# Optimization experiments

Measured on AMD Instinct MI355X. Metric: run time of the kernel, lower is better.

Reference implementation:

```python
import jax, jax.numpy as jnp
import numpy as np

DIM = 1024
TOPK = 64
PAIRS = DIM // 2  # phase_pairs default
PHASE_MIX = 0.5
GATE_THRESHOLD = 0.0
EPS = 1e-12  # F.normalize default eps


def _l2norm(v):
    # matches F.normalize(v, dim=-1): v / max(||v||, eps)
    n = jnp.linalg.norm(v, axis=-1, keepdims=True)
    return v / jnp.maximum(n, EPS)


def setup_inputs() -> dict:
    key = jax.random.key(0)
    ks = jax.random.split(key, 6)
    s = 0.02  # small init scale for weights
    return {
        "x": jax.random.normal(ks[0], (4, 4096, DIM), dtype=jnp.float32),
        "gate_W": jax.random.normal(ks[1], (DIM, DIM), dtype=jnp.float32) * s,
        "gate_b": jnp.zeros((DIM,), dtype=jnp.float32),
        "mag_W": jax.random.normal(ks[2], (DIM, DIM), dtype=jnp.float32) * s,
        "mag_b": jnp.zeros((DIM,), dtype=jnp.float32),
        "Wq": jax.random.normal(ks[3], (DIM, DIM), dtype=jnp.float32) * s,
        "Wk": jax.random.normal(ks[4], (DIM, DIM), dtype=jnp.float32) * s,
        "phase_W": jax.random.normal(ks[5], (2 * PAIRS, DIM), dtype=jnp.float32) * s,
    }


def reference(x, gate_W, gate_b, mag_W, mag_b, Wq, Wk, phase_W):
    B, S, D = x.shape
    # gated SAE-style projection (gated=True, diag=False)
    gate_pre = x @ gate_W.T + gate_b          # [B,S,D]
    mag_pre = x @ mag_W.T + mag_b             # [B,S,D]
    # hard gate with straight-through estimator
    gate_soft = jax.nn.sigmoid(gate_pre)
    gate_hard = (gate_pre > GATE_THRESHOLD).astype(x.dtype)
    gate = gate_hard + gate_soft - jax.lax.stop_gradient(gate_soft)
    mag = jax.nn.relu(mag_pre)
    # top-k scatter mask along feature dim
    idx = jax.lax.top_k(gate_pre, TOPK)[1]    # [B,S,K]
    rows = jnp.arange(B * S)[:, None]
    mask = (jnp.zeros((B * S, D), dtype=bool)
            .at[rows, idx.reshape(B * S, TOPK)].set(True)
            .reshape(B, S, D))
    gate = jnp.where(mask, gate, jnp.zeros_like(gate))
    mag = jnp.where(mask, mag, jnp.zeros_like(mag))
    xg = gate * mag
    # twist projections, L2-normalized
    q = _l2norm(xg @ Wq.T)
    k = _l2norm(xg @ Wk.T)
    # symplectic momentum map over consecutive steps
    momentum_map = q[:, 1:] * k[:, :-1] - q[:, :-1] * k[:, 1:]  # [B,S-1,D]
    twist_mag = jnp.linalg.norm(momentum_map, axis=-1, keepdims=True)
    complexity = jnp.pad(jnp.tanh(twist_mag), ((0, 0), (1, 0), (0, 0)))  # [B,S,1]
    # phase branch (phase_mix > 0)
    phase = (xg @ phase_W.T).reshape(B, S, PAIRS, 2)
    phase = _l2norm(phase)
    pp, pc = phase[:, :-1], phase[:, 1:]
    cross = pp[..., 0] * pc[..., 1] - pp[..., 1] * pc[..., 0]   # [B,S-1,P]
    dot = jnp.clip(jnp.sum(pp * pc, axis=-1), -1.0, 1.0)
    phase_delta = jnp.abs(jnp.arctan2(cross, dot)) / jnp.pi
    phase_score = jnp.pad(jnp.mean(phase_delta, axis=-1, keepdims=True),
                          ((0, 0), (1, 0), (0, 0)))             # [B,S,1]
    return (1.0 - PHASE_MIX) * complexity + PHASE_MIX * phase_score
```

## Files before the change

kernel.cpp:

```cpp
#include <hip/hip_runtime.h>
#include <math.h>

#define DIM 1024
#define ROWS 16384
#define SEQ 4096
#define MARGIN 0.012f
#define MAXC 24

typedef __bf16 v8bf __attribute__((ext_vector_type(8)));
typedef float v4f __attribute__((ext_vector_type(4)));
typedef int v8i __attribute__((ext_vector_type(8)));

__device__ __forceinline__ unsigned short f2bf(float f){
  unsigned u = __float_as_uint(f);
  u = u + 0x7FFFu + ((u >> 16) & 1u);
  return (unsigned short)(u >> 16);
}
__device__ __forceinline__ float bf2f(unsigned short h){
  return __uint_as_float(((unsigned)h) << 16);
}
__device__ __forceinline__ unsigned short relu_bf(unsigned short h){
  return (h & 0x8000u) ? (unsigned short)0 : h;
}
__device__ __forceinline__ unsigned f2fp8(float f){
  float a = fabsf(f);
  unsigned sign = (__float_as_uint(f) >> 24) & 0x80u;
  if (a >= 448.f) return sign | 0x7Eu;
  if (a < 0.015625f){
    int k = (int)rintf(a * 512.f);
    if (k >= 8) return sign | 0x08u;
    return sign | (unsigned)k;
  }
  unsigned u = __float_as_uint(a);
  u += 0x7FFFFu + ((u >> 20) & 1u);
  int e = (int)((u >> 23) & 0xFFu) - 127;
  unsigned m = (u >> 20) & 7u;
  if (e > 8) return sign | 0x7Eu;
  return sign | ((unsigned)(e + 7) << 3) | m;
}
__device__ __forceinline__ void lds_fence(){
  __asm__ volatile("s_waitcnt lgkmcnt(0)" ::: "memory");
}

__global__ __launch_bounds__(256) void cvt_all(
    const float* __restrict__ x,
    const float* __restrict__ w0, const float* __restrict__ w1,
    const float* __restrict__ w2, const float* __restrict__ w3,
    const float* __restrict__ w4,
    unsigned short* __restrict__ xbf, unsigned short* __restrict__ wbf,
    unsigned char* __restrict__ wf8){
  const int y = blockIdx.y;
  int i = (blockIdx.x * 256 + threadIdx.x) * 4;
  if (y < 16){
    const float* s = x + ((size_t)y << 20);
    float4 f = *(const float4*)(s + i);
    ushort4 o; o.x = f2bf(f.x); o.y = f2bf(f.y); o.z = f2bf(f.z); o.w = f2bf(f.w);
    *(ushort4*)(xbf + ((size_t)y << 20) + i) = o;
  } else if (y < 18){
    const float* s = (y == 16) ? w0 : w1;
    float4 f = *(const float4*)(s + i);
    ushort4 o; o.x = f2bf(f.x); o.y = f2bf(f.y); o.z = f2bf(f.z); o.w = f2bf(f.w);
    *(ushort4*)(wbf + ((size_t)(y - 16) << 20) + i) = o;
  } else {
    const float* s = (y == 18) ? w2 : ((y == 19) ? w3 : w4);
    float4 f = *(const float4*)(s + i);
    unsigned u = f2fp8(f.x * 32.f) | (f2fp8(f.y * 32.f) << 8) |
                 (f2fp8(f.z * 32.f) << 16) | (f2fp8(f.w * 32.f) << 24);
    *(unsigned*)(wf8 + ((size_t)(y - 18) << 20) + i) = u;
  }
}

#define GBAR() asm volatile("s_barrier" ::: "memory")
#define GLGKM0() { asm volatile("s_waitcnt lgkmcnt(0)" ::: "memory"); __builtin_amdgcn_sched_barrier(0); }
#define GVM4() asm volatile("s_waitcnt vmcnt(4)" ::: "memory")

__global__ __launch_bounds__(512, 2) void gemm_bt(
    const unsigned short* __restrict__ A, const unsigned short* __restrict__ B,
    const float* __restrict__ bias0, const float* __restrict__ bias1,
    unsigned short* __restrict__ C0, unsigned short* __restrict__ C1)
{
  extern __shared__ unsigned char lds[];
  const int t = threadIdx.x;
  const int lane = t & 63, wave = t >> 6;
  const int wr = wave >> 2, wc = wave & 3;
  const int bid = blockIdx.x;
  const int swz = (bid & 7) * 64 + (bid >> 3);
  const int m0 = (swz & 63) * 256;
  const int n0 = (swz >> 6) * 256;

  int offv[4];
#pragma unroll
  for (int h = 0; h < 2; h++)
#pragma unroll
    for (int i = 0; i < 2; i++){
      int o = h * 16384 + i * 8192 + t * 16;
      int u = o ^ (((o >> 9) & 1) << 5);
      int r = ((u >> 11) << 4) | ((u >> 6) & 15);
      int c = (((u >> 10) & 1) << 5) | ((u & 63) >> 1);
      offv[h * 2 + i] = r * 1024 + c;
    }
  const int off00 = offv[0], off01 = offv[1], off10 = offv[2], off11 = offv[3];
  const unsigned short* Ab = A + ((size_t)m0 << 10);
  const unsigned short* Bb = B + ((size_t)n0 << 10);

  const int laneterm = (lane & 15) * 64 + (((lane >> 4) * 16) ^ (((lane >> 3) & 1) * 32));
  const int aBase = wr * 16384 + laneterm;
  const int bBase = 32768 + wc * 8192 + laneterm;

#define GLD1(srcp, dsto) __builtin_amdgcn_global_load_lds( \
    (const __attribute__((address_space(1))) void*)(srcp), \
    (__attribute__((address_space(3))) void*)(lds + (dsto)), 16, 0, 0)

  auto stageA = [&](int h, int kt, int pp){
    const int o0 = h ? off10 : off00, o1 = h ? off11 : off01;
    GLD1(Ab + o0 + kt * 64, pp * 65536 + h * 16384 + t * 16);
    GLD1(Ab + o1 + kt * 64, pp * 65536 + h * 16384 + 8192 + t * 16);
  };
  auto stageB = [&](int h, int kt, int pp){
    const int o0 = h ? off10 : off00, o1 = h ? off11 : off01;
    GLD1(Bb + o0 + kt * 64, pp * 65536 + 32768 + h * 16384 + t * 16);
    GLD1(Bb + o1 + kt * 64, pp * 65536 + 32768 + h * 16384 + 8192 + t * 16);
  };

  v4f acc[8][4];
#pragma unroll
  for (int i = 0; i < 8; i++)
#pragma unroll
    for (int j = 0; j < 4; j++) acc[i][j] = v4f{0.f, 0.f, 0.f, 0.f};

  stageB(0, 0, 0); stageB(1, 0, 0);
  stageA(0, 0, 0); stageA(1, 0, 0);
  stageB(0, 1, 1); stageB(1, 1, 1);
  GVM4();
  GBAR();

  int p = 0;
  for (int X = 0; X < 16; X++, p ^= 1){
    const int pb = p * 65536;
    const int ktA = (X + 1 < 16) ? X + 1 : 15;
    const int ktB = (X + 2 < 16) ? X + 2 : X;
    v8bf a0[8], a1[8], b0[4], b1[4];

#pragma unroll
    for (int mi = 0; mi < 8; mi++) a0[mi] = *(const v8bf*)(lds + pb + aBase + mi * 2048);
#pragma unroll
    for (int ni = 0; ni < 4; ni++) b0[ni] = *(const v8bf*)(lds + pb + bBase + ni * 2048);
    stageA(0, ktA, p ^ 1);
    GBAR();
    __builtin_amdgcn_s_setprio(1);
#pragma unroll
    for (int mi = 0; mi < 4; mi++)
#pragma unroll
      for (int ni = 0; ni < 4; ni++)
        acc[mi][ni] = __builtin_amdgcn_mfma_f32_16x16x32_bf16(a0[mi], b0[ni], acc[mi][ni], 0, 0, 0);
    __builtin_amdgcn_s_setprio(0);
    GBAR();

#pragma unroll
    for (int mi = 0; mi < 4; mi++) a1[mi] = *(const v8bf*)(lds + pb + aBase + 1024 + mi * 2048);
#pragma unroll
    for (int ni = 0; ni < 4; ni++) b1[ni] = *(const v8bf*)(lds + pb + bBase + 1024 + ni * 2048);
    stageA(1, ktA, p ^ 1);
    GBAR();
    __builtin_amdgcn_s_setprio(1);
#pragma unroll
    for (int mi = 0; mi < 4; mi++)
#pragma unroll
      for (int ni = 0; ni < 4; ni++)
        acc[4 + mi][ni] = __builtin_amdgcn_mfma_f32_16x16x32_bf16(a0[4 + mi], b0[ni], acc[4 + mi][ni], 0, 0, 0);
    __builtin_amdgcn_s_setprio(0);
    GLGKM0();
    GBAR();

#pragma unroll
    for (int mi = 4; mi < 8; mi++) a1[mi] = *(const v8bf*)(lds + pb + aBase + 1024 + mi * 2048);
    stageB(0, ktB, p);
    GBAR();
    __builtin_amdgcn_s_setprio(1);
#pragma unroll
    for (int mi = 0; mi < 4; mi++)
#pragma unroll
      for (int ni = 0; ni < 4; ni++)
        acc[mi][ni] = __builtin_amdgcn_mfma_f32_16x16x32_bf16(a1[mi], b1[ni], acc[mi][ni], 0, 0, 0);
    __builtin_amdgcn_s_setprio(0);
    GBAR();

    stageB(1, ktB, p);
    GBAR();
    __builtin_amdgcn_s_setprio(1);
#pragma unroll
    for (int mi = 0; mi < 4; mi++)
#pragma unroll
      for (int ni = 0; ni < 4; ni++)
        acc[4 + mi][ni] = __builtin_amdgcn_mfma_f32_16x16x32_bf16(a1[4 + mi], b1[ni], acc[4 + mi][ni], 0, 0, 0);
    __builtin_amdgcn_s_setprio(0);
    GVM4();
    GBAR();
  }

  asm volatile("s_waitcnt vmcnt(0)" ::: "memory");
  __syncthreads();

  const int os = n0 >> 10;
  unsigned short* Cp = (os == 0) ? C0 : C1;
  const float* bp = (os == 0) ? bias0 : bias1;
  const int colbase = n0 & (DIM - 1);
  unsigned short* lt = (unsigned short*)lds;
  const int ar = lane & 15, aq = lane >> 4;
  const int lrw = wr * 16 + aq * 4;
  const int lrow = t >> 4;
  const int cseg = (t & 15) * 16;
  const size_t grb = (size_t)(m0 + (lrow >> 4) * 128 + (lrow & 15)) * DIM + colbase + cseg;
  float bv[4];
#pragma unroll
  for (int ni = 0; ni < 4; ni++) bv[ni] = bp[colbase + wc * 64 + ni * 16 + ar];
#pragma unroll
  for (int mi = 0; mi < 8; mi++){
#pragma unroll
    for (int ni = 0; ni < 4; ni++){
      const int colc = wc * 64 + ni * 16 + ar;
#pragma unroll
      for (int rr = 0; rr < 4; rr++)
        lt[(lrw + rr) * 264 + colc] = f2bf(acc[mi][ni][rr] + bv[ni]);
    }
    __syncthreads();
    uint4 v0 = *(const uint4*)&lt[lrow * 264 + cseg];
    uint4 v1 = *(const uint4*)&lt[lrow * 264 + cseg + 8];
    *(uint4*)(Cp + grb + (size_t)mi * 16 * DIM) = v0;
    *(uint4*)(Cp + grb + (size_t)mi * 16 * DIM + 8) = v1;
    __syncthreads();
  }
  asm volatile("s_waitcnt vmcnt(0)" ::: "memory");
}

__global__ __launch_bounds__(256, 3) void gemm8(
    const unsigned char* __restrict__ A, const unsigned char* __restrict__ B,
    unsigned short* __restrict__ C0, unsigned short* __restrict__ C1,
    unsigned short* __restrict__ C2)
{
  __shared__ unsigned char lA[128 * 128];
  __shared__ unsigned char lB[128 * 128];
  const int t = threadIdx.x;
  const int lane = t & 63, wave = t >> 6;
  const int bid0 = blockIdx.y * gridDim.x + blockIdx.x;
  const int swz = (bid0 & 7) * 384 + (bid0 >> 3);
  const int m0 = (swz & 127) * 128;
  const int n0 = (swz >> 7) * 128;
  const int wm = (wave >> 1) * 64, wn = (wave & 1) * 64;
  const int ar = lane & 15, aq = lane >> 4;

  v4f acc[4][4];
#pragma unroll
  for (int i = 0; i < 4; i++)
#pragma unroll
    for (int j = 0; j < 4; j++) acc[i][j] = v4f{0.f, 0.f, 0.f, 0.f};

  for (int k0 = 0; k0 < DIM; k0 += 128){
#pragma unroll
    for (int i = 0; i < 4; i++){
      int c = (wave * 4 + i) * 64 + lane;
      int row = c >> 3, kq = c & 7;
      __builtin_amdgcn_global_load_lds(
        (const __attribute__((address_space(1))) void*)(A + (size_t)(m0 + row) * DIM + k0 + kq * 16),
        (__attribute__((address_space(3))) void*)(&lA[c * 16]), 16, 0, 0);
      __builtin_amdgcn_global_load_lds(
        (const __attribute__((address_space(1))) void*)(B + (size_t)(n0 + row) * DIM + k0 + kq * 16),
        (__attribute__((address_space(3))) void*)(&lB[c * 16]), 16, 0, 0);
    }
    __syncthreads();
    v8i a8[4], b8[4];
#pragma unroll
    for (int i = 0; i < 4; i++){
      a8[i] = *(const v8i*)&lA[(wm + i * 16 + ar) * 128 + aq * 32];
      b8[i] = *(const v8i*)&lB[(wn + i * 16 + ar) * 128 + aq * 32];
    }
#pragma unroll
    for (int mi = 0; mi < 4; mi++)
#pragma unroll
      for (int ni = 0; ni < 4; ni++)
        acc[mi][ni] = __builtin_amdgcn_mfma_scale_f32_16x16x128_f8f6f4(
            a8[mi], b8[ni], acc[mi][ni], 0, 0, 0, 127u, 0, 127u);
    __syncthreads();
  }

  const int os = n0 >> 10;
  unsigned short* Cp = (os == 0) ? C0 : ((os == 1) ? C1 : C2);
  const int colbase = n0 & (DIM - 1);
  unsigned short* lt = (unsigned short*)lA;
  const int lrw = (wave >> 1) * 16 + aq * 4;
  const int colc0 = (wave & 1) * 64;
  const int lrow = t >> 3;
  const int cseg = (t & 7) * 16;
  const size_t grb = (size_t)(m0 + (lrow >> 4) * 64 + (lrow & 15)) * DIM + colbase + cseg;
#pragma unroll
  for (int mi = 0; mi < 4; mi++){
#pragma unroll
    for (int ni = 0; ni < 4; ni++){
      const int colc = colc0 + ni * 16 + ar;
#pragma unroll
      for (int rr = 0; rr < 4; rr++)
        lt[(lrw + rr) * 136 + colc] = f2bf(acc[mi][ni][rr] * 0.03125f);
    }
    __syncthreads();
    uint4 v0 = *(const uint4*)&lt[lrow * 136 + cseg];
    uint4 v1 = *(const uint4*)&lt[lrow * 136 + cseg + 8];
    *(uint4*)(Cp + grb + (size_t)mi * 16 * DIM) = v0;
    *(uint4*)(Cp + grb + (size_t)mi * 16 * DIM + 8) = v1;
    __syncthreads();
  }
}

__global__ __launch_bounds__(256) void select_k(
  const unsigned short* __restrict__ gate_pre, const unsigned short* __restrict__ mag_pre,
  const float* __restrict__ x, const float* __restrict__ gW, const float* __restrict__ gb,
  unsigned char* __restrict__ xg8)
{
  __shared__ int   s_cnt[4];
  __shared__ int   s_idx[4][MAXC];
  __shared__ float s_ex [4][MAXC];
  __shared__ int   s_res[4][MAXC];

  const int t = threadIdx.x;
  const int lane = t & 63, wave = t >> 6;
  const int r = blockIdx.x * 4 + wave;
  const size_t rb = (size_t)r * DIM;

  float vg[16], vx[16];
  unsigned short mg[16];
#pragma unroll
  for (int c = 0; c < 4; c++){
    ushort4 g4 = *(const ushort4*)(gate_pre + rb + c * 256 + lane * 4);
    float4 x4 = *(const float4*)(x          + rb + c * 256 + lane * 4);
    ushort4 m4 = *(const ushort4*)(mag_pre  + rb + c * 256 + lane * 4);
    vg[c*4+0]=bf2f(g4.x); vg[c*4+1]=bf2f(g4.y); vg[c*4+2]=bf2f(g4.z); vg[c*4+3]=bf2f(g4.w);
    vx[c*4+0]=x4.x; vx[c*4+1]=x4.y; vx[c*4+2]=x4.z; vx[c*4+3]=x4.w;
    mg[c*4+0]=m4.x; mg[c*4+1]=m4.y; mg[c*4+2]=m4.z; mg[c*4+3]=m4.w;
  }
  if (lane == 0) s_cnt[wave] = 0;

  float lo = -8.f, hi = 8.f;
#pragma unroll
  for (int it = 0; it < 15; it++){
    float mid = 0.5f * (lo + hi);
    int cn = 0;
#pragma unroll
    for (int e = 0; e < 16; e++) cn += (vg[e] > mid) ? 1 : 0;
#pragma unroll
    for (int m = 32; m; m >>= 1) cn += __shfl_xor(cn, m);
    if (cn >= 64) lo = mid; else hi = mid;
  }
  const float cl = lo - MARGIN, ch = hi + MARGIN;

  int n1 = 0;
#pragma unroll
  for (int e = 0; e < 16; e++) n1 += (vg[e] > ch) ? 1 : 0;
#pragma unroll
  for (int m = 32; m; m >>= 1) n1 += __shfl_xor(n1, m);
  const int s = 64 - n1;

  lds_fence();
#pragma unroll
  for (int e = 0; e < 16; e++){
    float vv = vg[e];
    if (vv >= cl && vv <= ch){
      int p = atomicAdd(&s_cnt[wave], 1);
      if (p < MAXC) s_idx[wave][p] = (e >> 2) * 256 + lane * 4 + (e & 3);
    }
  }
  lds_fence();
  int namb = s_cnt[wave]; if (namb > MAXC) namb = MAXC;

  for (int i = 0; i < namb; i++){
    int d = s_idx[wave][i];
    const float* wr = gW + (size_t)d * DIM;
    float p = 0.f;
#pragma unroll
    for (int c = 0; c < 4; c++){
      float4 w4 = *(const float4*)(wr + c * 256 + lane * 4);
      p = fmaf(vx[c*4+0], w4.x, p); p = fmaf(vx[c*4+1], w4.y, p);
      p = fmaf(vx[c*4+2], w4.z, p); p = fmaf(vx[c*4+3], w4.w, p);
    }
#pragma unroll
    for (int m = 32; m; m >>= 1) p += __shfl_xor(p, m);
    if (lane == 0) s_ex[wave][i] = p + gb[d];
  }
  lds_fence();

  if (lane < namb){
    float e = s_ex[wave][lane]; int d = s_idx[wave][lane];
    int rank = 0;
    for (int j = 0; j < namb; j++){
      float ej = s_ex[wave][j]; int dj = s_idx[wave][j];
      if (ej > e || (ej == e && dj < d)) rank++;
    }
    s_res[wave][lane] = (rank < s && e > 0.f) ? 1 : 0;
  }
  lds_fence();

  float vals[16];
#pragma unroll
  for (int e = 0; e < 16; e++)
    vals[e] = (vg[e] > ch && vg[e] > 0.f) ? bf2f(relu_bf(mg[e])) : 0.f;
  for (int i = 0; i < namb; i++){
    int d = s_idx[wave][i];
    int res = s_res[wave][i];
    if (((d >> 2) & 63) == lane){
      int e = (d >> 8) * 4 + (d & 3);
      vals[e] = res ? bf2f(relu_bf(mg[e])) : 0.f;
    }
  }
#pragma unroll
  for (int c = 0; c < 4; c++){
    unsigned u = f2fp8(vals[c*4+0]) | (f2fp8(vals[c*4+1]) << 8) |
                 (f2fp8(vals[c*4+2]) << 16) | (f2fp8(vals[c*4+3]) << 24);
    *(unsigned*)(xg8 + rb + c * 256 + lane * 4) = u;
  }
}

__global__ __launch_bounds__(256) void epilogue_k(
  const unsigned short* __restrict__ q_pre, const unsigned short* __restrict__ k_pre,
  const unsigned short* __restrict__ p_pre, float* __restrict__ out)
{
  const int r0 = blockIdx.x * 4;
  const int t = threadIdx.x;
  const int lane = t & 63, wave = t >> 6;
  __shared__ float red[16];

  const int rp = (r0 == 0) ? 0 : r0 - 1;
  float vqp[4], vkp[4], vpp[4];
  {
    ushort4 uq = *(const ushort4*)(q_pre + (size_t)rp * DIM + 4*t);
    ushort4 uk = *(const ushort4*)(k_pre + (size_t)rp * DIM + 4*t);
    ushort4 up = *(const ushort4*)(p_pre + (size_t)rp * DIM + 4*t);
    vqp[0]=bf2f(uq.x); vqp[1]=bf2f(uq.y); vqp[2]=bf2f(uq.z); vqp[3]=bf2f(uq.w);
    vkp[0]=bf2f(uk.x); vkp[1]=bf2f(uk.y); vkp[2]=bf2f(uk.z); vkp[3]=bf2f(uk.w);
    vpp[0]=bf2f(up.x); vpp[1]=bf2f(up.y); vpp[2]=bf2f(up.z); vpp[3]=bf2f(up.w);
  }
  float aq = 0.f, ak = 0.f;
#pragma unroll
  for (int j = 0; j < 4; j++){ aq = fmaf(vqp[j], vqp[j], aq); ak = fmaf(vkp[j], vkp[j], ak); }
#pragma unroll
  for (int m = 32; m; m >>= 1){ aq += __shfl_xor(aq, m); ak += __shfl_xor(ak, m); }
  if (lane == 0){ red[wave] = aq; red[4 + wave] = ak; }
  __syncthreads();
  float rqp = 1.f / fmaxf(sqrtf(red[0] + red[1] + red[2] + red[3]), 1e-12f);
  float rkp = 1.f / fmaxf(sqrtf(red[4] + red[5] + red[6] + red[7]), 1e-12f);
  __syncthreads();

  for (int rr = 0; rr < 4; rr++){
    const int r = r0 + rr;
    float vqc[4], vkc[4], vpc[4];
    {
      ushort4 uq = *(const ushort4*)(q_pre + (size_t)r * DIM + 4*t);
      ushort4 uk = *(const ushort4*)(k_pre + (size_t)r * DIM + 4*t);
      ushort4 up = *(const ushort4*)(p_pre + (size_t)r * DIM + 4*t);
      vqc[0]=bf2f(uq.x); vqc[1]=bf2f(uq.y); vqc[2]=bf2f(uq.z); vqc[3]=bf2f(uq.w);
      vkc[0]=bf2f(uk.x); vkc[1]=bf2f(uk.y); vkc[2]=bf2f(uk.z); vkc[3]=bf2f(uk.w);
      vpc[0]=bf2f(up.x); vpc[1]=bf2f(up.y); vpc[2]=bf2f(up.z); vpc[3]=bf2f(up.w);
    }
    const bool seg = (r & (SEQ - 1)) == 0;
    float aqc = 0.f, akc = 0.f;
#pragma unroll
    for (int j = 0; j < 4; j++){ aqc = fmaf(vqc[j], vqc[j], aqc); akc = fmaf(vkc[j], vkc[j], akc); }
    float dsum = 0.f;
    if (!seg){
#pragma unroll
      for (int j = 0; j < 2; j++){
        float ax = vpp[2*j], ay = vpp[2*j+1], bx = vpc[2*j], by = vpc[2*j+1];
        float ia = 1.f / fmaxf(sqrtf(ax * ax + ay * ay), 1e-12f);
        float ib = 1.f / fmaxf(sqrtf(bx * bx + by * by), 1e-12f);
        ax *= ia; ay *= ia; bx *= ib; by *= ib;
        float cross = ax * by - ay * bx;
        float dot = fminf(fmaxf(ax * bx + ay * by, -1.f), 1.f);
        dsum += fabsf(atan2f(cross, dot)) * 0.3183098861837907f;
      }
    }
#pragma unroll
    for (int m = 32; m; m >>= 1){
      aqc += __shfl_xor(aqc, m); akc += __shfl_xor(akc, m); dsum += __shfl_xor(dsum, m);
    }
    if (lane == 0){ red[wave] = aqc; red[4 + wave] = akc; red[8 + wave] = dsum; }
    __syncthreads();
    float rqc = 1.f / fmaxf(sqrtf(red[0] + red[1] + red[2] + red[3]), 1e-12f);
    float rkc = 1.f / fmaxf(sqrtf(red[4] + red[5] + red[6] + red[7]), 1e-12f);
    if (!seg){
      float tw = 0.f;
#pragma unroll
      for (int j = 0; j < 4; j++){
        float m = (vqc[j] * rqc) * (vkp[j] * rkp) - (vqp[j] * rqp) * (vkc[j] * rkc);
        tw = fmaf(m, m, tw);
      }
#pragma unroll
      for (int m = 32; m; m >>= 1) tw += __shfl_xor(tw, m);
      if (lane == 0) red[12 + wave] = tw;
      __syncthreads();
      if (t == 0){
        float dtot = red[8] + red[9] + red[10] + red[11];
        float twt = red[12] + red[13] + red[14] + red[15];
        out[r] = 0.5f * tanhf(sqrtf(twt)) + 0.5f * (dtot * (1.f / 512.f));
      }
    } else {
      if (t == 0) out[r] = 0.f;
    }
    __syncthreads();
#pragma unroll
    for (int j = 0; j < 4; j++){ vqp[j] = vqc[j]; vkp[j] = vkc[j]; vpp[j] = vpc[j]; }
    rqp = rqc; rkp = rkc;
  }
}

extern "C" void kernel_launch(void* const* d_in, const int* in_sizes, int n_in,
                              void* d_out, int out_size, void* d_ws, size_t ws_size,
                              hipStream_t stream)
{
  const float* x       = (const float*)d_in[0];
  const float* gate_W  = (const float*)d_in[1];
  const float* gate_b  = (const float*)d_in[2];
  const float* mag_W   = (const float*)d_in[3];
  const float* mag_b   = (const float*)d_in[4];
  const float* Wq      = (const float*)d_in[5];
  const float* Wk      = (const float*)d_in[6];
  const float* phase_W = (const float*)d_in[7];
  float* out = (float*)d_out;

  char* ws = (char*)d_ws;
  unsigned short* xbf = (unsigned short*)ws;
  unsigned short* wbf = (unsigned short*)(ws + 33554432);
  unsigned char*  wf8 = (unsigned char*)(ws + 37748736);
  unsigned short* gate_pre = (unsigned short*)(ws + 41943040);
  unsigned short* mag_pre  = (unsigned short*)(ws + 75497472);
  unsigned short* p_pre    = (unsigned short*)(ws + 109051904);
  unsigned short* q_pre = gate_pre;
  unsigned short* k_pre = mag_pre;

  static bool attr_set = false;
  if (!attr_set){
    hipFuncSetAttribute((const void*)gemm_bt,
                        hipFuncAttributeMaxDynamicSharedMemorySize, 131072);
    attr_set = true;
  }

  dim3 b256(256);
  cvt_all<<<dim3(1024, 21), b256, 0, stream>>>(x, gate_W, mag_W, Wq, Wk, phase_W,
                                               xbf, wbf, wf8);

  gemm_bt<<<dim3(512), dim3(512), 131072, stream>>>(xbf, wbf, gate_b, mag_b,
                                                    gate_pre, mag_pre);

  unsigned char* xg8 = (unsigned char*)xbf;
  select_k<<<ROWS / 4, b256, 0, stream>>>(gate_pre, mag_pre, x, gate_W, gate_b, xg8);

  gemm8<<<dim3(24, 128), b256, 0, stream>>>(xg8, wf8, q_pre, k_pre, p_pre);

  epilogue_k<<<ROWS / 4, b256, 0, stream>>>(q_pre, k_pre, p_pre, out);
}
```

Baseline: 395.4 us.

## Replace bisection top-k threshold with two-pass radix histogram select in select_k

The 15-iteration bisection threshold search (each step a wave-wide reduction) is replaced by a two-pass 8-bit radix histogram over order-preserving bf16 keys in LDS, giving an exact 64th-largest threshold. Loads are widened to 8 elements per lane, the gate-weight row loads for ambiguous candidates are software-prefetched one iteration ahead, and fp8 packing uses the hardware v_cvt_pk_fp8_f32 instruction. This cuts reduction latency and instruction count in the selection kernel, at the cost of LDS atomics and extra shared memory. It may also change rounding or behaviour relative to the old f2fp8 helper.

```diff
diff --git a/kernel.cpp b/kernel.cpp
--- a/kernel.cpp
+++ b/kernel.cpp
@@ -315,6 +315,7 @@
   const float* __restrict__ x, const float* __restrict__ gW, const float* __restrict__ gb,
   unsigned char* __restrict__ xg8)
 {
+  __shared__ int   s_h  [4][256];
   __shared__ int   s_cnt[4];
   __shared__ int   s_idx[4][MAXC];
   __shared__ float s_ex [4][MAXC];
@@ -322,34 +323,81 @@
 
   const int t = threadIdx.x;
   const int lane = t & 63, wave = t >> 6;
-  const int r = blockIdx.x * 4 + wave;
-  const size_t rb = (size_t)r * DIM;
-
-  float vg[16], vx[16];
-  unsigned short mg[16];
-#pragma unroll
-  for (int c = 0; c < 4; c++){
-    ushort4 g4 = *(const ushort4*)(gate_pre + rb + c * 256 + lane * 4);
-    float4 x4 = *(const float4*)(x          + rb + c * 256 + lane * 4);
-    ushort4 m4 = *(const ushort4*)(mag_pre  + rb + c * 256 + lane * 4);
-    vg[c*4+0]=bf2f(g4.x); vg[c*4+1]=bf2f(g4.y); vg[c*4+2]=bf2f(g4.z); vg[c*4+3]=bf2f(g4.w);
-    vx[c*4+0]=x4.x; vx[c*4+1]=x4.y; vx[c*4+2]=x4.z; vx[c*4+3]=x4.w;
-    mg[c*4+0]=m4.x; mg[c*4+1]=m4.y; mg[c*4+2]=m4.z; mg[c*4+3]=m4.w;
-  }
+  const int row = blockIdx.x * 4 + wave;
+  const size_t rb = (size_t)row * DIM;
+
+  uint4 ga = *(const uint4*)(gate_pre + rb + lane * 8);
+  uint4 gB = *(const uint4*)(gate_pre + rb + 512 + lane * 8);
+  float4 xa0 = *(const float4*)(x + rb + lane * 8);
+  float4 xa1 = *(const float4*)(x + rb + lane * 8 + 4);
+  float4 xb0 = *(const float4*)(x + rb + 512 + lane * 8);
+  float4 xb1 = *(const float4*)(x + rb + 512 + lane * 8 + 4);
+  uint4 ma = *(const uint4*)(mag_pre + rb + lane * 8);
+  uint4 mb = *(const uint4*)(mag_pre + rb + 512 + lane * 8);
+
+  unsigned gw[8] = {ga.x, ga.y, ga.z, ga.w, gB.x, gB.y, gB.z, gB.w};
+  unsigned mw[8] = {ma.x, ma.y, ma.z, ma.w, mb.x, mb.y, mb.z, mb.w};
+  float vg[16], vm[16];
+  unsigned kk[16];
+#pragma unroll
+  for (int j = 0; j < 8; j++){
+    unsigned w = gw[j];
+    vg[2*j]   = __uint_as_float(w << 16);
+    vg[2*j+1] = __uint_as_float(w & 0xFFFF0000u);
+    unsigned lo = w & 0xFFFFu, hi = w >> 16;
+    kk[2*j]   = (lo & 0x8000u) ? (~lo & 0xFFFFu) : (lo | 0x8000u);
+    kk[2*j+1] = (hi & 0x8000u) ? (~hi & 0xFFFFu) : (hi | 0x8000u);
+    unsigned m = mw[j];
+    vm[2*j]   = __uint_as_float(m << 16);
+    vm[2*j+1] = __uint_as_float(m & 0xFFFF0000u);
+  }
+  float vx[16] = {xa0.x, xa0.y, xa0.z, xa0.w, xa1.x, xa1.y, xa1.z, xa1.w,
+                  xb0.x, xb0.y, xb0.z, xb0.w, xb1.x, xb1.y, xb1.z, xb1.w};
+
   if (lane == 0) s_cnt[wave] = 0;
 
-  float lo = -8.f, hi = 8.f;
-#pragma unroll
-  for (int it = 0; it < 15; it++){
-    float mid = 0.5f * (lo + hi);
-    int cn = 0;
-#pragma unroll
-    for (int e = 0; e < 16; e++) cn += (vg[e] > mid) ? 1 : 0;
-#pragma unroll
-    for (int m = 32; m; m >>= 1) cn += __shfl_xor(cn, m);
-    if (cn >= 64) lo = mid; else hi = mid;
-  }
-  const float cl = lo - MARGIN, ch = hi + MARGIN;
+  auto findbin = [&](int rk, int &bout, int &Cout){
+    int c0 = s_h[wave][lane*4+0], c1 = s_h[wave][lane*4+1];
+    int c2 = s_h[wave][lane*4+2], c3 = s_h[wave][lane*4+3];
+    int sl = c0 + c1 + c2 + c3;
+    int tt = sl;
+#pragma unroll
+    for (int m = 1; m < 64; m <<= 1){
+      int u = __shfl(tt, lane + m);
+      if (lane + m < 64) tt += u;
+    }
+    int ab = tt - sl;
+    int bb = -1, CC = 0;
+    int a3 = ab;       if (a3 < rk && rk <= a3 + c3){ bb = lane*4+3; CC = a3; }
+    int a2 = ab + c3;  if (bb < 0 && a2 < rk && rk <= a2 + c2){ bb = lane*4+2; CC = a2; }
+    int a1 = a2 + c2;  if (bb < 0 && a1 < rk && rk <= a1 + c1){ bb = lane*4+1; CC = a1; }
+    int a0 = a1 + c1;  if (bb < 0 && a0 < rk && rk <= a0 + c0){ bb = lane*4+0; CC = a0; }
+    unsigned long long mk = __ballot(bb >= 0);
+    int src = (int)__ffsll(mk) - 1;
+    bout = __shfl(bb, src); Cout = __shfl(CC, src);
+  };
+
+  s_h[wave][lane*4+0] = 0; s_h[wave][lane*4+1] = 0;
+  s_h[wave][lane*4+2] = 0; s_h[wave][lane*4+3] = 0;
+  lds_fence();
+#pragma unroll
+  for (int e = 0; e < 16; e++) atomicAdd(&s_h[wave][kk[e] >> 8], 1);
+  lds_fence();
+  int b1, C1; findbin(64, b1, C1);
+
+  s_h[wave][lane*4+0] = 0; s_h[wave][lane*4+1] = 0;
+  s_h[wave][lane*4+2] = 0; s_h[wave][lane*4+3] = 0;
+  lds_fence();
+#pragma unroll
+  for (int e = 0; e < 16; e++)
+    if ((int)(kk[e] >> 8) == b1) atomicAdd(&s_h[wave][kk[e] & 255u], 1);
+  lds_fence();
+  int b2, C2; findbin(64 - C1, b2, C2);
+
+  unsigned tkey = ((unsigned)b1 << 8) | (unsigned)b2;
+  unsigned hthr = (tkey & 0x8000u) ? (tkey & 0x7FFFu) : (~tkey & 0xFFFFu);
+  const float thr = bf2f((unsigned short)hthr);
+  const float cl = thr - MARGIN, ch = thr + MARGIN;
 
   int n1 = 0;
 #pragma unroll
@@ -364,25 +412,43 @@
     float vv = vg[e];
     if (vv >= cl && vv <= ch){
       int p = atomicAdd(&s_cnt[wave], 1);
-      if (p < MAXC) s_idx[wave][p] = (e >> 2) * 256 + lane * 4 + (e & 3);
+      if (p < MAXC) s_idx[wave][p] = (e >> 3) * 512 + lane * 8 + (e & 7);
     }
   }
   lds_fence();
   int namb = s_cnt[wave]; if (namb > MAXC) namb = MAXC;
 
+  const int o0 = lane * 8, o1 = lane * 8 + 4, o2 = 512 + lane * 8, o3 = 512 + lane * 8 + 4;
+  float4 w0, w1, w2, w3;
+  int dcur = 0;
+  if (namb > 0){
+    dcur = s_idx[wave][0];
+    const float* wr0 = gW + (size_t)dcur * DIM;
+    w0 = *(const float4*)(wr0 + o0); w1 = *(const float4*)(wr0 + o1);
+    w2 = *(const float4*)(wr0 + o2); w3 = *(const float4*)(wr0 + o3);
+  }
   for (int i = 0; i < namb; i++){
-    int d = s_idx[wave][i];
-    const float* wr = gW + (size_t)d * DIM;
+    float4 c0 = w0, c1 = w1, c2 = w2, c3 = w3;
+    int dn = 0;
+    if (i + 1 < namb){
+      dn = s_idx[wave][i + 1];
+      const float* wr2 = gW + (size_t)dn * DIM;
+      w0 = *(const float4*)(wr2 + o0); w1 = *(const float4*)(wr2 + o1);
+      w2 = *(const float4*)(wr2 + o2); w3 = *(const float4*)(wr2 + o3);
+    }
     float p = 0.f;
-#pragma unroll
-    for (int c = 0; c < 4; c++){
-      float4 w4 = *(const float4*)(wr + c * 256 + lane * 4);
-      p = fmaf(vx[c*4+0], w4.x, p); p = fmaf(vx[c*4+1], w4.y, p);
-      p = fmaf(vx[c*4+2], w4.z, p); p = fmaf(vx[c*4+3], w4.w, p);
-    }
+    p = fmaf(vx[0], c0.x, p);  p = fmaf(vx[1], c0.y, p);
+    p = fmaf(vx[2], c0.z, p);  p = fmaf(vx[3], c0.w, p);
+    p = fmaf(vx[4], c1.x, p);  p = fmaf(vx[5], c1.y, p);
+    p = fmaf(vx[6], c1.z, p);  p = fmaf(vx[7], c1.w, p);
+    p = fmaf(vx[8], c2.x, p);  p = fmaf(vx[9], c2.y, p);
+    p = fmaf(vx[10], c2.z, p); p = fmaf(vx[11], c2.w, p);
+    p = fmaf(vx[12], c3.x, p); p = fmaf(vx[13], c3.y, p);
+    p = fmaf(vx[14], c3.z, p); p = fmaf(vx[15], c3.w, p);
 #pragma unroll
     for (int m = 32; m; m >>= 1) p += __shfl_xor(p, m);
-    if (lane == 0) s_ex[wave][i] = p + gb[d];
+    if (lane == 0) s_ex[wave][i] = p + gb[dcur];
+    dcur = dn;
   }
   lds_fence();
 
@@ -397,24 +463,37 @@
   }
   lds_fence();
 
-  float vals[16];
-#pragma unroll
-  for (int e = 0; e < 16; e++)
-    vals[e] = (vg[e] > ch && vg[e] > 0.f) ? bf2f(relu_bf(mg[e])) : 0.f;
+  unsigned inb = 0, rsm = 0;
   for (int i = 0; i < namb; i++){
     int d = s_idx[wave][i];
-    int res = s_res[wave][i];
-    if (((d >> 2) & 63) == lane){
-      int e = (d >> 8) * 4 + (d & 3);
-      vals[e] = res ? bf2f(relu_bf(mg[e])) : 0.f;
-    }
-  }
-#pragma unroll
-  for (int c = 0; c < 4; c++){
-    unsigned u = f2fp8(vals[c*4+0]) | (f2fp8(vals[c*4+1]) << 8) |
-                 (f2fp8(vals[c*4+2]) << 16) | (f2fp8(vals[c*4+3]) << 24);
-    *(unsigned*)(xg8 + rb + c * 256 + lane * 4) = u;
-  }
+    if (((d & 511) >> 3) == lane){
+      int e = (d >> 9) * 8 + (d & 7);
+      inb |= 1u << e;
+      if (s_res[wave][i]) rsm |= 1u << e;
+    }
+  }
+
+  float vals[16];
+#pragma unroll
+  for (int e = 0; e < 16; e++){
+    float mv = (vm[e] > 0.f) ? vm[e] : 0.f;
+    float v = (vg[e] > ch && vg[e] > 0.f) ? mv : 0.f;
+    if ((inb >> e) & 1u) v = ((rsm >> e) & 1u) ? mv : 0.f;
+    vals[e] = v;
+  }
+
+  unsigned pk[4];
+#pragma unroll
+  for (int q = 0; q < 4; q++){
+    unsigned a = 0, b = 0;
+    asm volatile("v_cvt_pk_fp8_f32 %0, %1, %2" : "+v"(a) : "v"(vals[4*q+0]), "v"(vals[4*q+1]));
+    asm volatile("v_cvt_pk_fp8_f32 %0, %1, %2" : "+v"(b) : "v"(vals[4*q+2]), "v"(vals[4*q+3]));
+    pk[q] = (a & 0xFFFFu) | (b << 16);
+  }
+  uint2 st0; st0.x = pk[0]; st0.y = pk[1];
+  uint2 st1; st1.x = pk[2]; st1.y = pk[3];
+  *(uint2*)(xg8 + rb + lane * 8) = st0;
+  *(uint2*)(xg8 + rb + 512 + lane * 8) = st1;
 }
 
 __global__ __launch_bounds__(256) void epilogue_k(
```

Result: faster. 382.6 us (-3.2%).
